# Optimization experiments

Hardware: AMD Instinct MI355X
Metric: run time of the kernel (lower is better)

Reference implementation:

```python
import jax, jax.numpy as jnp
import numpy as np

N_ROI, N_GRAPHS, HID, EDIM, EMB, NGRP = 116, 128, 64, 5, 16, 4
IN_CH, OUT_CH, N_LAYERS = 116, 2, 2


def _seg_softmax(scores, seg, num_segments):
    # numerically stable softmax over edges grouped by target node
    m = jax.ops.segment_max(scores, seg, num_segments=num_segments)
    ex = jnp.exp(scores - m[seg])
    s = jax.ops.segment_sum(ex, seg, num_segments=num_segments)
    return ex / (s[seg] + 1e-16)


def setup_inputs():
    key = jax.random.key(0)
    ks = jax.random.split(key, 16)
    N = N_ROI * N_GRAPHS
    idx = np.arange(N_ROI)
    s = np.repeat(idx, N_ROI)
    d = np.tile(idx, N_ROI)
    off = (np.arange(N_GRAPHS) * N_ROI)[:, None]
    src = (s[None, :] + off).reshape(-1)
    dst = (d[None, :] + off).reshape(-1)
    E = src.size

    def W(i, shp):
        fan = shp[-2] if len(shp) >= 2 else shp[-1]
        return jax.random.normal(ks[i], shp, jnp.float32) / np.sqrt(fan)

    def z(*shp):
        return jnp.zeros(shp, jnp.float32)

    return {
        "x": jax.random.normal(ks[0], (N, IN_CH), jnp.float32),
        "edge_attr": jax.random.normal(ks[1], (E, EDIM), jnp.float32),
        "emb": W(2, (NGRP, EMB)),
        "enc_W": W(3, (IN_CH + EMB, HID)), "enc_b": z(HID),
        "bn_g": jnp.ones((HID,), jnp.float32), "bn_b": z(HID),
        "gine_We": W(4, (EDIM, HID)), "gine_be": z(HID),
        "gine_W1": W(5, (HID, HID)), "gine_b1": z(HID),
        "gine_W2": W(6, (HID, HID)), "gine_b2": z(HID),
        "gat_Wl": W(7, (N_LAYERS, HID, HID)), "gat_bl": z(N_LAYERS, HID),
        "gat_Wr": W(8, (N_LAYERS, HID, HID)), "gat_br": z(N_LAYERS, HID),
        "gat_att": W(9, (N_LAYERS, HID)),
        "gat_We": W(10, (N_LAYERS, EDIM, HID)),
        "gat_bias": z(N_LAYERS, HID),
        "pool_W1": W(11, (HID, HID)), "pool_b1": z(HID), "pool_w2": W(12, (HID,)),
        "lin1_W": W(13, (HID, IN_CH)), "lin1_b": z(IN_CH),
        "lin2_W": W(14, (IN_CH, OUT_CH)), "lin2_b": z(OUT_CH),
        "edge_index": jnp.asarray(np.stack([src, dst]), jnp.int32),
        "batch": jnp.asarray(np.repeat(np.arange(N_GRAPHS), N_ROI), jnp.int32),
        "group_ids": jnp.asarray(np.tile(idx // 29, N_GRAPHS), jnp.int32),
        "num_graphs": N_GRAPHS,
    }


def reference(x, edge_attr, emb, enc_W, enc_b, bn_g, bn_b,
              gine_We, gine_be, gine_W1, gine_b1, gine_W2, gine_b2,
              gat_Wl, gat_bl, gat_Wr, gat_br, gat_att, gat_We, gat_bias,
              pool_W1, pool_b1, pool_w2, lin1_W, lin1_b, lin2_W, lin2_b,
              edge_index, batch, group_ids, num_graphs):
    src, dst = edge_index[0], edge_index[1]
    N = x.shape[0]
    # BrainEncodeEmbed: concat group embedding, linear, batchnorm (batch stats)
    h = jnp.concatenate([x, emb[group_ids]], axis=-1)          # [N, IN_CH+EMB]
    h = jax.nn.relu(h @ enc_W + enc_b)                          # [N, HID]
    mu = h.mean(0)
    var = h.var(0)
    h = (h - mu) * jax.lax.rsqrt(var + 1e-5) * bn_g + bn_b
    # GINEConv (eps=0): sum_j relu(x_j + lin_edge(e_ij)), then MLP
    e = edge_attr @ gine_We + gine_be                           # [E, HID]
    agg = jax.ops.segment_sum(jax.nn.relu(h[src] + e), dst, num_segments=N)
    h = h + agg
    h = jax.nn.relu(h @ gine_W1 + gine_b1) @ gine_W2 + gine_b2
    h = jax.nn.relu(h)
    # GATv2 layers (heads=1, concat=False)
    for l in range(N_LAYERS):
        xl = h @ gat_Wl[l] + gat_bl[l]                          # [N, HID]
        xr = h @ gat_Wr[l] + gat_br[l]
        zed = jax.nn.leaky_relu(xl[src] + xr[dst] + edge_attr @ gat_We[l], 0.2)
        alpha = _seg_softmax(zed @ gat_att[l], dst, N)          # [E]
        h = jax.nn.relu(
            jax.ops.segment_sum(xl[src] * alpha[:, None], dst, num_segments=N)
            + gat_bias[l])
    # AttentionPooling: global softmax over all nodes, scatter-add by graph
    w = jax.nn.softmax(jnp.tanh(h @ pool_W1 + pool_b1) @ pool_w2, axis=0)
    pooled = jax.ops.segment_sum(h * w[:, None], batch, num_segments=num_graphs)
    return jax.nn.relu(pooled @ lin1_W + lin1_b) @ lin2_W + lin2_b
```

## Files before the change

kernel.cpp:

```cpp
#include <hip/hip_runtime.h>
#include <math.h>

#define R    116
#define R2   (116*116)
#define G    128
#define NN   (R*G)
#define HID  64
#define EDIM 5
#define INCH 116
#define EMBD 16

__device__ __forceinline__ float waveReduceSum(float v) {
#pragma unroll
    for (int m = 32; m >= 1; m >>= 1) v += __shfl_xor(v, m, 64);
    return v;
}

__device__ __forceinline__ float rlane(float v, int i) {
    return __int_as_float(__builtin_amdgcn_readlane(__float_as_int(v), i));
}

__global__ __launch_bounds__(256) void k_etr(
    const float* __restrict__ ea, float* __restrict__ eat) {
    int b = blockIdx.x;
    int g = b >> 4;
    int t = b & 15;
    int i0 = (t >> 2) << 5, j0 = (t & 3) << 5;
    int ni = min(32, R - i0), nj = min(32, R - j0);
    __shared__ float tile[32][165];
    const float* src = ea + ((size_t)(g*R + i0)*R + j0)*EDIM;
    int tot = ni * nj * EDIM;
    for (int idx = threadIdx.x; idx < tot; idx += 256) {
        int ii = idx / (nj*EDIM);
        int rem = idx - ii*(nj*EDIM);
        tile[ii][rem] = src[(size_t)ii*R*EDIM + rem];
    }
    __syncthreads();
    float* dst = eat + ((size_t)(g*R + j0)*R + i0)*EDIM;
    int tot2 = nj * ni * EDIM;
    for (int idx = threadIdx.x; idx < tot2; idx += 256) {
        int jj = idx / (ni*EDIM);
        int rem = idx - jj*(ni*EDIM);
        int ii = rem / EDIM, e = rem - ii*EDIM;
        dst[(size_t)jj*R*EDIM + rem] = tile[ii][jj*EDIM + e];
    }
}

__global__ __launch_bounds__(64) void k_prep(
    const float* __restrict__ We, const float* __restrict__ att,
    float* __restrict__ wepack, float* __restrict__ was2) {
    int l = blockIdx.x, c = threadIdx.x;
    const float* Wl = We + l*EDIM*HID;
    const float* al = att + l*HID;
    float g0=Wl[c], g1=Wl[64+c], g2=Wl[128+c], g3=Wl[192+c], g4=Wl[256+c];
    float at = al[c];
    float* wp = wepack + l*HID*8 + c*8;
    wp[0]=g0; wp[1]=g1; wp[2]=g2; wp[3]=g3; wp[4]=g4; wp[5]=at;
    wp[6]=0.f; wp[7]=0.f;
    float p0 = waveReduceSum(g0*at);
    float p1 = waveReduceSum(g1*at);
    float p2 = waveReduceSum(g2*at);
    float p3 = waveReduceSum(g3*at);
    float p4 = waveReduceSum(g4*at);
    if (c == 0) {
        float* ws = was2 + l*8;
        ws[0]=p0; ws[1]=p1; ws[2]=p2; ws[3]=p3; ws[4]=p4;
    }
}

__global__ __launch_bounds__(256) void k_encode(
    const float* __restrict__ x, const float* __restrict__ emb,
    const int* __restrict__ group_ids,
    const float* __restrict__ W, const float* __restrict__ bvec,
    float* __restrict__ h) {
    int w = threadIdx.x >> 6, lane = threadIdx.x & 63;
    int n = blockIdx.x*4 + w;
    __shared__ float xin[4][136];
    for (int idx = lane; idx < INCH; idx += 64) xin[w][idx] = x[(size_t)n*INCH + idx];
    if (lane < EMBD) xin[w][INCH + lane] = emb[group_ids[n]*EMBD + lane];
    float acc = bvec[lane];
#pragma unroll
    for (int k = 0; k < INCH + EMBD; k += 4) {
        float4 q = *(const float4*)&xin[w][k];
        acc = fmaf(q.x, W[(k  )*HID + lane], acc);
        acc = fmaf(q.y, W[(k+1)*HID + lane], acc);
        acc = fmaf(q.z, W[(k+2)*HID + lane], acc);
        acc = fmaf(q.w, W[(k+3)*HID + lane], acc);
    }
    h[(size_t)n*HID + lane] = fmaxf(acc, 0.f);
}

__global__ __launch_bounds__(256) void k_stats_partial(
    const float* __restrict__ h, float* __restrict__ partials) {
    int b = blockIdx.x;
    int tid = threadIdx.x;
    int c = tid & 63, r0 = tid >> 6;
    float s = 0.f, s2 = 0.f;
    int row0 = b*64;
#pragma unroll
    for (int k = 0; k < 16; ++k) {
        float v = h[(size_t)(row0 + r0 + 4*k)*HID + c];
        s += v; s2 += v*v;
    }
    __shared__ float ls[256], l2[256];
    ls[tid] = s; l2[tid] = s2;
    __syncthreads();
    if (tid < 64) {
        s  = ls[tid] + ls[tid+64] + ls[tid+128] + ls[tid+192];
        s2 = l2[tid] + l2[tid+64] + l2[tid+128] + l2[tid+192];
        partials[b*128 + tid]      = s;
        partials[b*128 + 64 + tid] = s2;
    }
}

__global__ __launch_bounds__(64) void k_stats_final(
    const float* __restrict__ partials, const float* __restrict__ gam,
    const float* __restrict__ bet, float* __restrict__ stats) {
    int c = threadIdx.x;
    float s = 0.f, s2 = 0.f;
    for (int b = 0; b < NN/64; ++b) {
        s  += partials[b*128 + c];
        s2 += partials[b*128 + 64 + c];
    }
    float mu  = s / (float)NN;
    float var = s2 / (float)NN - mu*mu;
    float rs  = rsqrtf(var + 1e-5f);
    float sc  = rs * gam[c];
    stats[c]      = sc;
    stats[64 + c] = bet[c] - mu*sc;
}

__global__ __launch_bounds__(256) void k_gine(
    const float* __restrict__ h, const float* __restrict__ stats,
    const float* __restrict__ eat,
    const float* __restrict__ We, const float* __restrict__ be,
    const float* __restrict__ W1, const float* __restrict__ b1,
    const float* __restrict__ W2, const float* __restrict__ b2,
    float* __restrict__ hout) {
    int b = blockIdx.x;
    int g = b & (G-1), chunk = b >> 7;
    int tid = threadIdx.x, w = tid >> 6, lane = tid & 63;
    int j = chunk*4 + w;
    __shared__ float eac[4][R*8];
    __shared__ float t1s[4][68];
    size_t hbase = (size_t)g*R*HID;
    float scv = stats[lane], shv = stats[64 + lane];
    const float* col = eat + (size_t)(g*R + j)*R*EDIM;
    for (int idx = lane; idx < R*EDIM; idx += 64) {
        int i = idx / EDIM, e = idx - i*EDIM;
        eac[w][i*8 + e] = col[idx];
    }
    float w0=We[lane], w1v=We[64+lane], w2v=We[128+lane],
          w3v=We[192+lane], w4v=We[256+lane], bec=be[lane];
    const float* hg = h + hbase;
    float agg = 0.f;
#pragma unroll 4
    for (int i = 0; i < R; ++i) {
        float4 q = *(const float4*)&eac[w][i*8];
        float q4 = eac[w][i*8 + 4];
        float hv = fmaf(hg[(size_t)i*HID + lane], scv, shv);
        float ew = bec;
        ew = fmaf(q.x, w0,  ew); ew = fmaf(q.y, w1v, ew);
        ew = fmaf(q.z, w2v, ew); ew = fmaf(q.w, w3v, ew);
        ew = fmaf(q4,  w4v, ew);
        agg += fmaxf(hv + ew, 0.f);
    }
    float h1 = fmaf(hg[(size_t)j*HID + lane], scv, shv) + agg;
    t1s[w][lane] = h1;
    float a1 = b1[lane];
#pragma unroll
    for (int k = 0; k < HID; k += 4) {
        float4 tq = *(const float4*)&t1s[w][k];
        a1 = fmaf(tq.x, W1[(k  )*HID + lane], a1);
        a1 = fmaf(tq.y, W1[(k+1)*HID + lane], a1);
        a1 = fmaf(tq.z, W1[(k+2)*HID + lane], a1);
        a1 = fmaf(tq.w, W1[(k+3)*HID + lane], a1);
    }
    t1s[w][lane] = fmaxf(a1, 0.f);
    float a2 = b2[lane];
#pragma unroll
    for (int k = 0; k < HID; k += 4) {
        float4 tq = *(const float4*)&t1s[w][k];
        a2 = fmaf(tq.x, W2[(k  )*HID + lane], a2);
        a2 = fmaf(tq.y, W2[(k+1)*HID + lane], a2);
        a2 = fmaf(tq.z, W2[(k+2)*HID + lane], a2);
        a2 = fmaf(tq.w, W2[(k+3)*HID + lane], a2);
    }
    hout[hbase + (size_t)j*HID + lane] = fmaxf(a2, 0.f);
}

__global__ __launch_bounds__(256) void k_xlxr(
    const float* __restrict__ h,
    const float* __restrict__ Wl, const float* __restrict__ bl,
    const float* __restrict__ Wr, const float* __restrict__ br,
    const float* __restrict__ att,
    float* __restrict__ xl, float* __restrict__ xr,
    float* __restrict__ axl, float* __restrict__ axr) {
    int w = threadIdx.x >> 6, lane = threadIdx.x & 63;
    int n = blockIdx.x*4 + w;
    __shared__ float hr[4][68];
    hr[w][lane] = h[(size_t)n*HID + lane];
    float aL = bl[lane], aR = br[lane];
#pragma unroll
    for (int k = 0; k < HID; k += 4) {
        float4 q = *(const float4*)&hr[w][k];
        aL = fmaf(q.x, Wl[(k  )*HID + lane], aL);
        aR = fmaf(q.x, Wr[(k  )*HID + lane], aR);
        aL = fmaf(q.y, Wl[(k+1)*HID + lane], aL);
        aR = fmaf(q.y, Wr[(k+1)*HID + lane], aR);
        aL = fmaf(q.z, Wl[(k+2)*HID + lane], aL);
        aR = fmaf(q.z, Wr[(k+2)*HID + lane], aR);
        aL = fmaf(q.w, Wl[(k+3)*HID + lane], aL);
        aR = fmaf(q.w, Wr[(k+3)*HID + lane], aR);
    }
    xl[(size_t)n*HID + lane] = aL;
    xr[(size_t)n*HID + lane] = aR;
    float at = att[lane];
    float pL = waveReduceSum(aL * at);
    float pR = waveReduceSum(aR * at);
    if (lane == 0) { axl[n] = pL; axr[n] = pR; }
}

__global__ __launch_bounds__(256) void k_gat(
    const float* __restrict__ xl, const float* __restrict__ xr,
    const float* __restrict__ axlg, const float* __restrict__ axrg,
    const float* __restrict__ eat, const float* __restrict__ wepack,
    const float* __restrict__ wasg, const float* __restrict__ bias,
    float* __restrict__ hout) {
    int b = blockIdx.x;
    int g = b & (G-1), chunk = b >> 7;
    int j0c = chunk*15, jcnt = min(15, R - j0c);
    int tid = threadIdx.x, w = tid >> 6, lane = tid & 63;
    __shared__ float xls[R][66];
    size_t hbase = (size_t)g*R*HID;
    for (int idx = tid; idx < R*HID; idx += 256)
        xls[idx>>6][idx&63] = xl[hbase + idx];
    float biasv = bias[lane];
    float wasv0 = wasg[0], wasv1 = wasg[1], wasv2 = wasg[2],
          wasv3 = wasg[3], wasv4 = wasg[4];
    bool vB = lane < (R - 64);
    int rb = vB ? (64 + lane) : lane;
    float axA = axlg[g*R + lane];
    float axB = axlg[g*R + rb];
    __syncthreads();

    for (int p = 0; p < 2; ++p) {
        int jj0 = w + 8*p, jj1 = w + 4 + 8*p;
        bool act0 = jj0 < jcnt, act1 = jj1 < jcnt;
        int j0 = j0c + (act0 ? jj0 : 0);
        int j1 = j0c + (act1 ? jj1 : 0);
        const float* c0 = eat + (size_t)(g*R + j0)*R*EDIM;
        const float* c1 = eat + (size_t)(g*R + j1)*R*EDIM;
        float e0A[5], e0B[5], e1A[5], e1B[5];
#pragma unroll
        for (int e = 0; e < 5; ++e) {
            e0A[e] = c0[lane*EDIM + e];  e0B[e] = c0[rb*EDIM + e];
            e1A[e] = c1[lane*EDIM + e];  e1B[e] = c1[rb*EDIM + e];
        }
        int xo0 = __builtin_amdgcn_readfirstlane(j0*HID);
        int xo1 = __builtin_amdgcn_readfirstlane(j1*HID);
        const float* xr0 = xr + hbase + xo0;
        const float* xr1 = xr + hbase + xo1;
        float axr0 = axrg[g*R + j0];
        float axr1 = axrg[g*R + j1];
        float acc0A=0.f, acc0B=0.f, acc1A=0.f, acc1B=0.f;
#pragma unroll 4
        for (int c = 0; c < HID; c += 2) {
            float2 xA2 = *(const float2*)&xls[lane][c];
            float2 xB2 = *(const float2*)&xls[rb][c];
            const float* wpa = wepack + c*8;
            const float* wpb = wepack + (c+1)*8;
            float u0a = xr0[c], u0b = xr0[c+1];
            float u1a = xr1[c], u1b = xr1[c+1];
            {
                float zA = xA2.x + u0a;
                zA = fmaf(e0A[0],wpa[0],zA); zA = fmaf(e0A[1],wpa[1],zA);
                zA = fmaf(e0A[2],wpa[2],zA); zA = fmaf(e0A[3],wpa[3],zA);
                zA = fmaf(e0A[4],wpa[4],zA);
                acc0A = fmaf(__builtin_fabsf(zA), wpa[5], acc0A);
                float zB = xB2.x + u0a;
                zB = fmaf(e0B[0],wpa[0],zB); zB = fmaf(e0B[1],wpa[1],zB);
                zB = fmaf(e0B[2],wpa[2],zB); zB = fmaf(e0B[3],wpa[3],zB);
                zB = fmaf(e0B[4],wpa[4],zB);
                acc0B = fmaf(__builtin_fabsf(zB), wpa[5], acc0B);
                float yA = xA2.x + u1a;
                yA = fmaf(e1A[0],wpa[0],yA); yA = fmaf(e1A[1],wpa[1],yA);
                yA = fmaf(e1A[2],wpa[2],yA); yA = fmaf(e1A[3],wpa[3],yA);
                yA = fmaf(e1A[4],wpa[4],yA);
                acc1A = fmaf(__builtin_fabsf(yA), wpa[5], acc1A);
                float yB = xB2.x + u1a;
                yB = fmaf(e1B[0],wpa[0],yB); yB = fmaf(e1B[1],wpa[1],yB);
                yB = fmaf(e1B[2],wpa[2],yB); yB = fmaf(e1B[3],wpa[3],yB);
                yB = fmaf(e1B[4],wpa[4],yB);
                acc1B = fmaf(__builtin_fabsf(yB), wpa[5], acc1B);
            }
            {
                float zA = xA2.y + u0b;
                zA = fmaf(e0A[0],wpb[0],zA); zA = fmaf(e0A[1],wpb[1],zA);
                zA = fmaf(e0A[2],wpb[2],zA); zA = fmaf(e0A[3],wpb[3],zA);
                zA = fmaf(e0A[4],wpb[4],zA);
                acc0A = fmaf(__builtin_fabsf(zA), wpb[5], acc0A);
                float zB = xB2.y + u0b;
                zB = fmaf(e0B[0],wpb[0],zB); zB = fmaf(e0B[1],wpb[1],zB);
                zB = fmaf(e0B[2],wpb[2],zB); zB = fmaf(e0B[3],wpb[3],zB);
                zB = fmaf(e0B[4],wpb[4],zB);
                acc0B = fmaf(__builtin_fabsf(zB), wpb[5], acc0B);
                float yA = xA2.y + u1b;
                yA = fmaf(e1A[0],wpb[0],yA); yA = fmaf(e1A[1],wpb[1],yA);
                yA = fmaf(e1A[2],wpb[2],yA); yA = fmaf(e1A[3],wpb[3],yA);
                yA = fmaf(e1A[4],wpb[4],yA);
                acc1A = fmaf(__builtin_fabsf(yA), wpb[5], acc1A);
                float yB = xB2.y + u1b;
                yB = fmaf(e1B[0],wpb[0],yB); yB = fmaf(e1B[1],wpb[1],yB);
                yB = fmaf(e1B[2],wpb[2],yB); yB = fmaf(e1B[3],wpb[3],yB);
                yB = fmaf(e1B[4],wpb[4],yB);
                acc1B = fmaf(__builtin_fabsf(yB), wpb[5], acc1B);
            }
        }
        float L0A = axA + axr0, L0B = axB + axr0;
        L0A = fmaf(e0A[0],wasv0,L0A); L0A = fmaf(e0A[1],wasv1,L0A);
        L0A = fmaf(e0A[2],wasv2,L0A); L0A = fmaf(e0A[3],wasv3,L0A);
        L0A = fmaf(e0A[4],wasv4,L0A);
        L0B = fmaf(e0B[0],wasv0,L0B); L0B = fmaf(e0B[1],wasv1,L0B);
        L0B = fmaf(e0B[2],wasv2,L0B); L0B = fmaf(e0B[3],wasv3,L0B);
        L0B = fmaf(e0B[4],wasv4,L0B);
        float L1A = axA + axr1, L1B = axB + axr1;
        L1A = fmaf(e1A[0],wasv0,L1A); L1A = fmaf(e1A[1],wasv1,L1A);
        L1A = fmaf(e1A[2],wasv2,L1A); L1A = fmaf(e1A[3],wasv3,L1A);
        L1A = fmaf(e1A[4],wasv4,L1A);
        L1B = fmaf(e1B[0],wasv0,L1B); L1B = fmaf(e1B[1],wasv1,L1B);
        L1B = fmaf(e1B[2],wasv2,L1B); L1B = fmaf(e1B[3],wasv3,L1B);
        L1B = fmaf(e1B[4],wasv4,L1B);
        float s0A = fmaf(0.4f, acc0A, 0.6f*L0A);
        float s0B = vB ? fmaf(0.4f, acc0B, 0.6f*L0B) : -1e30f;
        float m0 = fmaxf(s0A, s0B);
#pragma unroll
        for (int k = 32; k >= 1; k >>= 1) m0 = fmaxf(m0, __shfl_xor(m0, k, 64));
        float x0A = __expf(s0A - m0);
        float x0B = vB ? __expf(s0B - m0) : 0.f;
        float sm0 = x0A + x0B;
#pragma unroll
        for (int k = 32; k >= 1; k >>= 1) sm0 += __shfl_xor(sm0, k, 64);
        float inv0 = 1.f / (sm0 + 1e-16f);
        float p0A = x0A * inv0, p0B = x0B * inv0;

        float s1A = fmaf(0.4f, acc1A, 0.6f*L1A);
        float s1B = vB ? fmaf(0.4f, acc1B, 0.6f*L1B) : -1e30f;
        float m1 = fmaxf(s1A, s1B);
#pragma unroll
        for (int k = 32; k >= 1; k >>= 1) m1 = fmaxf(m1, __shfl_xor(m1, k, 64));
        float x1A = __expf(s1A - m1);
        float x1B = vB ? __expf(s1B - m1) : 0.f;
        float sm1 = x1A + x1B;
#pragma unroll
        for (int k = 32; k >= 1; k >>= 1) sm1 += __shfl_xor(sm1, k, 64);
        float inv1 = 1.f / (sm1 + 1e-16f);
        float p1A = x1A * inv1, p1B = x1B * inv1;

        float o0 = 0.f, o1 = 0.f;
#pragma unroll 8
        for (int i = 0; i < 64; ++i) {
            float xv = xls[i][lane];
            o0 = fmaf(rlane(p0A, i), xv, o0);
            o1 = fmaf(rlane(p1A, i), xv, o1);
        }
#pragma unroll 4
        for (int i = 0; i < R-64; ++i) {
            float xv = xls[64+i][lane];
            o0 = fmaf(rlane(p0B, i), xv, o0);
            o1 = fmaf(rlane(p1B, i), xv, o1);
        }
        if (act0) hout[hbase + (size_t)j0*HID + lane] = fmaxf(o0 + biasv, 0.f);
        if (act1) hout[hbase + (size_t)j1*HID + lane] = fmaxf(o1 + biasv, 0.f);
    }
}

__global__ __launch_bounds__(256) void k_pool_score(
    const float* __restrict__ h, const float* __restrict__ W1,
    const float* __restrict__ b1, const float* __restrict__ w2,
    float* __restrict__ scores) {
    int w = threadIdx.x >> 6, lane = threadIdx.x & 63;
    int n = blockIdx.x*4 + w;
    __shared__ float hr[4][68];
    hr[w][lane] = h[(size_t)n*HID + lane];
    float acc = b1[lane];
#pragma unroll
    for (int k = 0; k < HID; k += 4) {
        float4 q = *(const float4*)&hr[w][k];
        acc = fmaf(q.x, W1[(k  )*HID + lane], acc);
        acc = fmaf(q.y, W1[(k+1)*HID + lane], acc);
        acc = fmaf(q.z, W1[(k+2)*HID + lane], acc);
        acc = fmaf(q.w, W1[(k+3)*HID + lane], acc);
    }
    float p = tanhf(acc) * w2[lane];
    p = waveReduceSum(p);
    if (lane == 0) scores[n] = p;
}

__global__ __launch_bounds__(1024) void k_pool_reduce(
    const float* __restrict__ scores, float* __restrict__ ms) {
    __shared__ float red[1024];
    int tid = threadIdx.x;
    float m = -1e30f;
    for (int i = tid; i < NN; i += 1024) m = fmaxf(m, scores[i]);
    red[tid] = m;
    __syncthreads();
    for (int s = 512; s > 0; s >>= 1) {
        if (tid < s) red[tid] = fmaxf(red[tid], red[tid+s]);
        __syncthreads();
    }
    float mx = red[0];
    __syncthreads();
    float sum = 0.f;
    for (int i = tid; i < NN; i += 1024) sum += __expf(scores[i] - mx);
    red[tid] = sum;
    __syncthreads();
    for (int s = 512; s > 0; s >>= 1) {
        if (tid < s) red[tid] += red[tid+s];
        __syncthreads();
    }
    if (tid == 0) { ms[0] = mx; ms[1] = red[0]; }
}

__global__ __launch_bounds__(64) void k_pool_final(
    const float* __restrict__ h, const float* __restrict__ scores,
    const float* __restrict__ ms,
    const float* __restrict__ lin1W, const float* __restrict__ lin1b,
    const float* __restrict__ lin2W, const float* __restrict__ lin2b,
    float* __restrict__ out) {
    int g = blockIdx.x, c = threadIdx.x;
    float mx = ms[0], inv = 1.f / ms[1];
    float pc = 0.f;
    int nb = g*R;
    for (int r = 0; r < R; ++r) {
        float wv = __expf(scores[nb + r] - mx) * inv;
        pc = fmaf(h[(size_t)(nb + r)*HID + c], wv, pc);
    }
    __shared__ float pl[HID];
    __shared__ float t[INCH];
    pl[c] = pc;
    __syncthreads();
    for (int k = c; k < INCH; k += 64) {
        float acc = lin1b[k];
#pragma unroll 8
        for (int q = 0; q < HID; ++q) acc = fmaf(pl[q], lin1W[q*INCH + k], acc);
        t[k] = fmaxf(acc, 0.f);
    }
    __syncthreads();
    if (c < 2) {
        float o = lin2b[c];
        for (int k = 0; k < INCH; ++k) o = fmaf(t[k], lin2W[k*2 + c], o);
        out[g*2 + c] = o;
    }
}

extern "C" void kernel_launch(void* const* d_in, const int* in_sizes, int n_in,
                              void* d_out, int out_size, void* d_ws, size_t ws_size,
                              hipStream_t stream) {
    (void)in_sizes; (void)n_in; (void)out_size; (void)ws_size;
    const float* x        = (const float*)d_in[0];
    const float* edge_attr= (const float*)d_in[1];
    const float* emb      = (const float*)d_in[2];
    const float* enc_W    = (const float*)d_in[3];
    const float* enc_b    = (const float*)d_in[4];
    const float* bn_g     = (const float*)d_in[5];
    const float* bn_b     = (const float*)d_in[6];
    const float* gine_We  = (const float*)d_in[7];
    const float* gine_be  = (const float*)d_in[8];
    const float* gine_W1  = (const float*)d_in[9];
    const float* gine_b1  = (const float*)d_in[10];
    const float* gine_W2  = (const float*)d_in[11];
    const float* gine_b2  = (const float*)d_in[12];
    const float* gat_Wl   = (const float*)d_in[13];
    const float* gat_bl   = (const float*)d_in[14];
    const float* gat_Wr   = (const float*)d_in[15];
    const float* gat_br   = (const float*)d_in[16];
    const float* gat_att  = (const float*)d_in[17];
    const float* gat_We   = (const float*)d_in[18];
    const float* gat_bias = (const float*)d_in[19];
    const float* pool_W1  = (const float*)d_in[20];
    const float* pool_b1  = (const float*)d_in[21];
    const float* pool_w2  = (const float*)d_in[22];
    const float* lin1_W   = (const float*)d_in[23];
    const float* lin1_b   = (const float*)d_in[24];
    const float* lin2_W   = (const float*)d_in[25];
    const float* lin2_b   = (const float*)d_in[26];
    const int*   group_ids= (const int*)d_in[29];
    float* out = (float*)d_out;

    float* w = (float*)d_ws;
    float* eat      = w;
    float* hA       = eat + (size_t)R2*G*EDIM;
    float* hB       = hA + (size_t)NN*HID;
    float* xlb      = hB + (size_t)NN*HID;
    float* xrb      = xlb + (size_t)NN*HID;
    float* axl      = xrb + (size_t)NN*HID;
    float* axr      = axl + NN;
    float* scores   = axr + NN;
    float* partials = scores + NN;
    float* stats    = partials + (NN/64)*128;
    float* pms      = stats + 128;
    float* wepack   = pms + 2;
    float* was2     = wepack + 2*HID*8;

    k_etr<<<G*16, 256, 0, stream>>>(edge_attr, eat);
    k_prep<<<2, 64, 0, stream>>>(gat_We, gat_att, wepack, was2);
    k_encode<<<NN/4, 256, 0, stream>>>(x, emb, group_ids, enc_W, enc_b, hA);
    k_stats_partial<<<NN/64, 256, 0, stream>>>(hA, partials);
    k_stats_final<<<1, 64, 0, stream>>>(partials, bn_g, bn_b, stats);
    k_gine<<<G*29, 256, 0, stream>>>(hA, stats, eat, gine_We, gine_be,
                                     gine_W1, gine_b1, gine_W2, gine_b2, hB);
    k_xlxr<<<NN/4, 256, 0, stream>>>(hB, gat_Wl, gat_bl, gat_Wr, gat_br,
                                     gat_att, xlb, xrb, axl, axr);
    k_gat<<<G*8, 256, 0, stream>>>(xlb, xrb, axl, axr, eat, wepack,
                                   was2, gat_bias, hA);
    k_xlxr<<<NN/4, 256, 0, stream>>>(hA, gat_Wl + HID*HID, gat_bl + HID,
                                     gat_Wr + HID*HID, gat_br + HID,
                                     gat_att + HID, xlb, xrb, axl, axr);
    k_gat<<<G*8, 256, 0, stream>>>(xlb, xrb, axl, axr, eat, wepack + HID*8,
                                   was2 + 8, gat_bias + HID, hB);
    k_pool_score<<<NN/4, 256, 0, stream>>>(hB, pool_W1, pool_b1, pool_w2, scores);
    k_pool_reduce<<<1, 1024, 0, stream>>>(scores, pms);
    k_pool_final<<<G, 64, 0, stream>>>(hB, scores, pms, lin1_W, lin1_b,
                                       lin2_W, lin2_b, out);
}
```

Before: 258.6 us.

## Fuse per-node projections into GINE and GAT epilogues, widen GAT blocks

Folds the GATv2 xl/xr projections and attention dot products into the epilogue of the GINE kernel and the first GAT kernel, and folds the pooling score computation into the second GAT kernel. This removes three standalone per-node kernels and their global read of h. GAT blocks move from 256 to 512 threads, with each wave handling two targets in one pass instead of looping. Double-buffered xl/xr arrays avoid read/write hazards between layers, at the cost of more workspace and register pressure in the fused kernels.

```diff
diff --git a/kernel.cpp b/kernel.cpp
--- a/kernel.cpp
+++ b/kernel.cpp
@@ -130,13 +130,18 @@
     stats[64 + c] = bet[c] - mu*sc;
 }
 
-__global__ __launch_bounds__(256) void k_gine(
+__global__ __launch_bounds__(256) void k_gine_x(
     const float* __restrict__ h, const float* __restrict__ stats,
     const float* __restrict__ eat,
     const float* __restrict__ We, const float* __restrict__ be,
     const float* __restrict__ W1, const float* __restrict__ b1,
     const float* __restrict__ W2, const float* __restrict__ b2,
-    float* __restrict__ hout) {
+    float* __restrict__ hout,
+    const float* __restrict__ Wl, const float* __restrict__ bl,
+    const float* __restrict__ Wr, const float* __restrict__ br,
+    const float* __restrict__ att,
+    float* __restrict__ oxl, float* __restrict__ oxr,
+    float* __restrict__ oaxl, float* __restrict__ oaxr) {
     int b = blockIdx.x;
     int g = b & (G-1), chunk = b >> 7;
     int tid = threadIdx.x, w = tid >> 6, lane = tid & 63;
@@ -186,24 +191,13 @@
         a2 = fmaf(tq.z, W2[(k+2)*HID + lane], a2);
         a2 = fmaf(tq.w, W2[(k+3)*HID + lane], a2);
     }
-    hout[hbase + (size_t)j*HID + lane] = fmaxf(a2, 0.f);
-}
-
-__global__ __launch_bounds__(256) void k_xlxr(
-    const float* __restrict__ h,
-    const float* __restrict__ Wl, const float* __restrict__ bl,
-    const float* __restrict__ Wr, const float* __restrict__ br,
-    const float* __restrict__ att,
-    float* __restrict__ xl, float* __restrict__ xr,
-    float* __restrict__ axl, float* __restrict__ axr) {
-    int w = threadIdx.x >> 6, lane = threadIdx.x & 63;
-    int n = blockIdx.x*4 + w;
-    __shared__ float hr[4][68];
-    hr[w][lane] = h[(size_t)n*HID + lane];
+    float hr = fmaxf(a2, 0.f);
+    hout[hbase + (size_t)j*HID + lane] = hr;
+    t1s[w][lane] = hr;
     float aL = bl[lane], aR = br[lane];
 #pragma unroll
     for (int k = 0; k < HID; k += 4) {
-        float4 q = *(const float4*)&hr[w][k];
+        float4 q = *(const float4*)&t1s[w][k];
         aL = fmaf(q.x, Wl[(k  )*HID + lane], aL);
         aR = fmaf(q.x, Wr[(k  )*HID + lane], aR);
         aL = fmaf(q.y, Wl[(k+1)*HID + lane], aL);
@@ -213,27 +207,35 @@
         aL = fmaf(q.w, Wl[(k+3)*HID + lane], aL);
         aR = fmaf(q.w, Wr[(k+3)*HID + lane], aR);
     }
-    xl[(size_t)n*HID + lane] = aL;
-    xr[(size_t)n*HID + lane] = aR;
+    oxl[hbase + (size_t)j*HID + lane] = aL;
+    oxr[hbase + (size_t)j*HID + lane] = aR;
     float at = att[lane];
     float pL = waveReduceSum(aL * at);
     float pR = waveReduceSum(aR * at);
-    if (lane == 0) { axl[n] = pL; axr[n] = pR; }
-}
-
-__global__ __launch_bounds__(256) void k_gat(
+    if (lane == 0) { oaxl[g*R + j] = pL; oaxr[g*R + j] = pR; }
+}
+
+template<int MODE>
+__global__ __launch_bounds__(512) void k_gat_x(
     const float* __restrict__ xl, const float* __restrict__ xr,
     const float* __restrict__ axlg, const float* __restrict__ axrg,
     const float* __restrict__ eat, const float* __restrict__ wepack,
     const float* __restrict__ wasg, const float* __restrict__ bias,
-    float* __restrict__ hout) {
+    float* __restrict__ hout,
+    const float* __restrict__ WA, const float* __restrict__ bA,
+    const float* __restrict__ WB, const float* __restrict__ bB,
+    const float* __restrict__ attv,
+    float* __restrict__ oxl, float* __restrict__ oxr,
+    float* __restrict__ oaxl, float* __restrict__ oaxr,
+    float* __restrict__ oscores) {
     int b = blockIdx.x;
     int g = b & (G-1), chunk = b >> 7;
     int j0c = chunk*15, jcnt = min(15, R - j0c);
     int tid = threadIdx.x, w = tid >> 6, lane = tid & 63;
     __shared__ float xls[R][66];
+    __shared__ float tt[8][68];
     size_t hbase = (size_t)g*R*HID;
-    for (int idx = tid; idx < R*HID; idx += 256)
+    for (int idx = tid; idx < R*HID; idx += 512)
         xls[idx>>6][idx&63] = xl[hbase + idx];
     float biasv = bias[lane];
     float wasv0 = wasg[0], wasv1 = wasg[1], wasv2 = wasg[2],
@@ -244,157 +246,177 @@
     float axB = axlg[g*R + rb];
     __syncthreads();
 
-    for (int p = 0; p < 2; ++p) {
-        int jj0 = w + 8*p, jj1 = w + 4 + 8*p;
-        bool act0 = jj0 < jcnt, act1 = jj1 < jcnt;
-        int j0 = j0c + (act0 ? jj0 : 0);
-        int j1 = j0c + (act1 ? jj1 : 0);
-        const float* c0 = eat + (size_t)(g*R + j0)*R*EDIM;
-        const float* c1 = eat + (size_t)(g*R + j1)*R*EDIM;
-        float e0A[5], e0B[5], e1A[5], e1B[5];
-#pragma unroll
-        for (int e = 0; e < 5; ++e) {
-            e0A[e] = c0[lane*EDIM + e];  e0B[e] = c0[rb*EDIM + e];
-            e1A[e] = c1[lane*EDIM + e];  e1B[e] = c1[rb*EDIM + e];
+    int jj0 = w, jj1 = w + 8;
+    bool act0 = jj0 < jcnt, act1 = jj1 < jcnt;
+    int j0 = j0c + (act0 ? jj0 : 0);
+    int j1 = j0c + (act1 ? jj1 : 0);
+    const float* c0 = eat + (size_t)(g*R + j0)*R*EDIM;
+    const float* c1 = eat + (size_t)(g*R + j1)*R*EDIM;
+    float e0A[5], e0B[5], e1A[5], e1B[5];
+#pragma unroll
+    for (int e = 0; e < 5; ++e) {
+        e0A[e] = c0[lane*EDIM + e];  e0B[e] = c0[rb*EDIM + e];
+        e1A[e] = c1[lane*EDIM + e];  e1B[e] = c1[rb*EDIM + e];
+    }
+    int xo0 = __builtin_amdgcn_readfirstlane(j0*HID);
+    int xo1 = __builtin_amdgcn_readfirstlane(j1*HID);
+    const float* xr0 = xr + hbase + xo0;
+    const float* xr1 = xr + hbase + xo1;
+    float axr0 = axrg[g*R + j0];
+    float axr1 = axrg[g*R + j1];
+    float acc0A=0.f, acc0B=0.f, acc1A=0.f, acc1B=0.f;
+#pragma unroll 4
+    for (int c = 0; c < HID; c += 2) {
+        float2 xA2 = *(const float2*)&xls[lane][c];
+        float2 xB2 = *(const float2*)&xls[rb][c];
+        const float* wpa = wepack + c*8;
+        const float* wpb = wepack + (c+1)*8;
+        float u0a = xr0[c], u0b = xr0[c+1];
+        float u1a = xr1[c], u1b = xr1[c+1];
+        {
+            float zA = xA2.x + u0a;
+            zA = fmaf(e0A[0],wpa[0],zA); zA = fmaf(e0A[1],wpa[1],zA);
+            zA = fmaf(e0A[2],wpa[2],zA); zA = fmaf(e0A[3],wpa[3],zA);
+            zA = fmaf(e0A[4],wpa[4],zA);
+            acc0A = fmaf(__builtin_fabsf(zA), wpa[5], acc0A);
+            float zB = xB2.x + u0a;
+            zB = fmaf(e0B[0],wpa[0],zB); zB = fmaf(e0B[1],wpa[1],zB);
+            zB = fmaf(e0B[2],wpa[2],zB); zB = fmaf(e0B[3],wpa[3],zB);
+            zB = fmaf(e0B[4],wpa[4],zB);
+            acc0B = fmaf(__builtin_fabsf(zB), wpa[5], acc0B);
+            float yA = xA2.x + u1a;
+            yA = fmaf(e1A[0],wpa[0],yA); yA = fmaf(e1A[1],wpa[1],yA);
+            yA = fmaf(e1A[2],wpa[2],yA); yA = fmaf(e1A[3],wpa[3],yA);
+            yA = fmaf(e1A[4],wpa[4],yA);
+            acc1A = fmaf(__builtin_fabsf(yA), wpa[5], acc1A);
+            float yB = xB2.x + u1a;
+            yB = fmaf(e1B[0],wpa[0],yB); yB = fmaf(e1B[1],wpa[1],yB);
+            yB = fmaf(e1B[2],wpa[2],yB); yB = fmaf(e1B[3],wpa[3],yB);
+            yB = fmaf(e1B[4],wpa[4],yB);
+            acc1B = fmaf(__builtin_fabsf(yB), wpa[5], acc1B);
         }
-        int xo0 = __builtin_amdgcn_readfirstlane(j0*HID);
-        int xo1 = __builtin_amdgcn_readfirstlane(j1*HID);
-        const float* xr0 = xr + hbase + xo0;
-        const float* xr1 = xr + hbase + xo1;
-        float axr0 = axrg[g*R + j0];
-        float axr1 = axrg[g*R + j1];
-        float acc0A=0.f, acc0B=0.f, acc1A=0.f, acc1B=0.f;
+        {
+            float zA = xA2.y + u0b;
+            zA = fmaf(e0A[0],wpb[0],zA); zA = fmaf(e0A[1],wpb[1],zA);
+            zA = fmaf(e0A[2],wpb[2],zA); zA = fmaf(e0A[3],wpb[3],zA);
+            zA = fmaf(e0A[4],wpb[4],zA);
+            acc0A = fmaf(__builtin_fabsf(zA), wpb[5], acc0A);
+            float zB = xB2.y + u0b;
+            zB = fmaf(e0B[0],wpb[0],zB); zB = fmaf(e0B[1],wpb[1],zB);
+            zB = fmaf(e0B[2],wpb[2],zB); zB = fmaf(e0B[3],wpb[3],zB);
+            zB = fmaf(e0B[4],wpb[4],zB);
+            acc0B = fmaf(__builtin_fabsf(zB), wpb[5], acc0B);
+            float yA = xA2.y + u1b;
+            yA = fmaf(e1A[0],wpb[0],yA); yA = fmaf(e1A[1],wpb[1],yA);
+            yA = fmaf(e1A[2],wpb[2],yA); yA = fmaf(e1A[3],wpb[3],yA);
+            yA = fmaf(e1A[4],wpb[4],yA);
+            acc1A = fmaf(__builtin_fabsf(yA), wpb[5], acc1A);
+            float yB = xB2.y + u1b;
+            yB = fmaf(e1B[0],wpb[0],yB); yB = fmaf(e1B[1],wpb[1],yB);
+            yB = fmaf(e1B[2],wpb[2],yB); yB = fmaf(e1B[3],wpb[3],yB);
+            yB = fmaf(e1B[4],wpb[4],yB);
+            acc1B = fmaf(__builtin_fabsf(yB), wpb[5], acc1B);
+        }
+    }
+    float L0A = axA + axr0, L0B = axB + axr0;
+    L0A = fmaf(e0A[0],wasv0,L0A); L0A = fmaf(e0A[1],wasv1,L0A);
+    L0A = fmaf(e0A[2],wasv2,L0A); L0A = fmaf(e0A[3],wasv3,L0A);
+    L0A = fmaf(e0A[4],wasv4,L0A);
+    L0B = fmaf(e0B[0],wasv0,L0B); L0B = fmaf(e0B[1],wasv1,L0B);
+    L0B = fmaf(e0B[2],wasv2,L0B); L0B = fmaf(e0B[3],wasv3,L0B);
+    L0B = fmaf(e0B[4],wasv4,L0B);
+    float L1A = axA + axr1, L1B = axB + axr1;
+    L1A = fmaf(e1A[0],wasv0,L1A); L1A = fmaf(e1A[1],wasv1,L1A);
+    L1A = fmaf(e1A[2],wasv2,L1A); L1A = fmaf(e1A[3],wasv3,L1A);
+    L1A = fmaf(e1A[4],wasv4,L1A);
+    L1B = fmaf(e1B[0],wasv0,L1B); L1B = fmaf(e1B[1],wasv1,L1B);
+    L1B = fmaf(e1B[2],wasv2,L1B); L1B = fmaf(e1B[3],wasv3,L1B);
+    L1B = fmaf(e1B[4],wasv4,L1B);
+    float s0A = fmaf(0.4f, acc0A, 0.6f*L0A);
+    float s0B = vB ? fmaf(0.4f, acc0B, 0.6f*L0B) : -1e30f;
+    float m0 = fmaxf(s0A, s0B);
+#pragma unroll
+    for (int k = 32; k >= 1; k >>= 1) m0 = fmaxf(m0, __shfl_xor(m0, k, 64));
+    float x0A = __expf(s0A - m0);
+    float x0B = vB ? __expf(s0B - m0) : 0.f;
+    float sm0 = x0A + x0B;
+#pragma unroll
+    for (int k = 32; k >= 1; k >>= 1) sm0 += __shfl_xor(sm0, k, 64);
+    float inv0 = 1.f / (sm0 + 1e-16f);
+    float p0A = x0A * inv0, p0B = x0B * inv0;
+
+    float s1A = fmaf(0.4f, acc1A, 0.6f*L1A);
+    float s1B = vB ? fmaf(0.4f, acc1B, 0.6f*L1B) : -1e30f;
+    float m1 = fmaxf(s1A, s1B);
+#pragma unroll
+    for (int k = 32; k >= 1; k >>= 1) m1 = fmaxf(m1, __shfl_xor(m1, k, 64));
+    float x1A = __expf(s1A - m1);
+    float x1B = vB ? __expf(s1B - m1) : 0.f;
+    float sm1 = x1A + x1B;
+#pragma unroll
+    for (int k = 32; k >= 1; k >>= 1) sm1 += __shfl_xor(sm1, k, 64);
+    float inv1 = 1.f / (sm1 + 1e-16f);
+    float p1A = x1A * inv1, p1B = x1B * inv1;
+
+    float o0 = 0.f, o1 = 0.f;
+#pragma unroll 8
+    for (int i = 0; i < 64; ++i) {
+        float xv = xls[i][lane];
+        o0 = fmaf(rlane(p0A, i), xv, o0);
+        o1 = fmaf(rlane(p1A, i), xv, o1);
+    }
 #pragma unroll 4
-        for (int c = 0; c < HID; c += 2) {
-            float2 xA2 = *(const float2*)&xls[lane][c];
-            float2 xB2 = *(const float2*)&xls[rb][c];
-            const float* wpa = wepack + c*8;
-            const float* wpb = wepack + (c+1)*8;
-            float u0a = xr0[c], u0b = xr0[c+1];
-            float u1a = xr1[c], u1b = xr1[c+1];
-            {
-                float zA = xA2.x + u0a;
-                zA = fmaf(e0A[0],wpa[0],zA); zA = fmaf(e0A[1],wpa[1],zA);
-                zA = fmaf(e0A[2],wpa[2],zA); zA = fmaf(e0A[3],wpa[3],zA);
-                zA = fmaf(e0A[4],wpa[4],zA);
-                acc0A = fmaf(__builtin_fabsf(zA), wpa[5], acc0A);
-                float zB = xB2.x + u0a;
-                zB = fmaf(e0B[0],wpa[0],zB); zB = fmaf(e0B[1],wpa[1],zB);
-                zB = fmaf(e0B[2],wpa[2],zB); zB = fmaf(e0B[3],wpa[3],zB);
-                zB = fmaf(e0B[4],wpa[4],zB);
-                acc0B = fmaf(__builtin_fabsf(zB), wpa[5], acc0B);
-                float yA = xA2.x + u1a;
-                yA = fmaf(e1A[0],wpa[0],yA); yA = fmaf(e1A[1],wpa[1],yA);
-                yA = fmaf(e1A[2],wpa[2],yA); yA = fmaf(e1A[3],wpa[3],yA);
-                yA = fmaf(e1A[4],wpa[4],yA);
-                acc1A = fmaf(__builtin_fabsf(yA), wpa[5], acc1A);
-                float yB = xB2.x + u1a;
-                yB = fmaf(e1B[0],wpa[0],yB); yB = fmaf(e1B[1],wpa[1],yB);
-                yB = fmaf(e1B[2],wpa[2],yB); yB = fmaf(e1B[3],wpa[3],yB);
-                yB = fmaf(e1B[4],wpa[4],yB);
-                acc1B = fmaf(__builtin_fabsf(yB), wpa[5], acc1B);
+    for (int i = 0; i < R-64; ++i) {
+        float xv = xls[64+i][lane];
+        o0 = fmaf(rlane(p0B, i), xv, o0);
+        o1 = fmaf(rlane(p1B, i), xv, o1);
+    }
+    float hr0 = fmaxf(o0 + biasv, 0.f);
+    float hr1 = fmaxf(o1 + biasv, 0.f);
+
+#pragma unroll
+    for (int t = 0; t < 2; ++t) {
+        bool act = t ? act1 : act0;
+        if (!act) continue;
+        int j = t ? j1 : j0;
+        float hr = t ? hr1 : hr0;
+        hout[hbase + (size_t)j*HID + lane] = hr;
+        tt[w][lane] = hr;
+        if (MODE == 0) {
+            float aL = bA[lane], aR = bB[lane];
+#pragma unroll
+            for (int k = 0; k < HID; k += 4) {
+                float4 q = *(const float4*)&tt[w][k];
+                aL = fmaf(q.x, WA[(k  )*HID + lane], aL);
+                aR = fmaf(q.x, WB[(k  )*HID + lane], aR);
+                aL = fmaf(q.y, WA[(k+1)*HID + lane], aL);
+                aR = fmaf(q.y, WB[(k+1)*HID + lane], aR);
+                aL = fmaf(q.z, WA[(k+2)*HID + lane], aL);
+                aR = fmaf(q.z, WB[(k+2)*HID + lane], aR);
+                aL = fmaf(q.w, WA[(k+3)*HID + lane], aL);
+                aR = fmaf(q.w, WB[(k+3)*HID + lane], aR);
             }
-            {
-                float zA = xA2.y + u0b;
-                zA = fmaf(e0A[0],wpb[0],zA); zA = fmaf(e0A[1],wpb[1],zA);
-                zA = fmaf(e0A[2],wpb[2],zA); zA = fmaf(e0A[3],wpb[3],zA);
-                zA = fmaf(e0A[4],wpb[4],zA);
-                acc0A = fmaf(__builtin_fabsf(zA), wpb[5], acc0A);
-                float zB = xB2.y + u0b;
-                zB = fmaf(e0B[0],wpb[0],zB); zB = fmaf(e0B[1],wpb[1],zB);
-                zB = fmaf(e0B[2],wpb[2],zB); zB = fmaf(e0B[3],wpb[3],zB);
-                zB = fmaf(e0B[4],wpb[4],zB);
-                acc0B = fmaf(__builtin_fabsf(zB), wpb[5], acc0B);
-                float yA = xA2.y + u1b;
-                yA = fmaf(e1A[0],wpb[0],yA); yA = fmaf(e1A[1],wpb[1],yA);
-                yA = fmaf(e1A[2],wpb[2],yA); yA = fmaf(e1A[3],wpb[3],yA);
-                yA = fmaf(e1A[4],wpb[4],yA);
-                acc1A = fmaf(__builtin_fabsf(yA), wpb[5], acc1A);
-                float yB = xB2.y + u1b;
-                yB = fmaf(e1B[0],wpb[0],yB); yB = fmaf(e1B[1],wpb[1],yB);
-                yB = fmaf(e1B[2],wpb[2],yB); yB = fmaf(e1B[3],wpb[3],yB);
-                yB = fmaf(e1B[4],wpb[4],yB);
-                acc1B = fmaf(__builtin_fabsf(yB), wpb[5], acc1B);
+            oxl[hbase + (size_t)j*HID + lane] = aL;
+            oxr[hbase + (size_t)j*HID + lane] = aR;
+            float at = attv[lane];
+            float pL = waveReduceSum(aL * at);
+            float pR = waveReduceSum(aR * at);
+            if (lane == 0) { oaxl[g*R + j] = pL; oaxr[g*R + j] = pR; }
+        } else {
+            float acc = bA[lane];
+#pragma unroll
+            for (int k = 0; k < HID; k += 4) {
+                float4 q = *(const float4*)&tt[w][k];
+                acc = fmaf(q.x, WA[(k  )*HID + lane], acc);
+                acc = fmaf(q.y, WA[(k+1)*HID + lane], acc);
+                acc = fmaf(q.z, WA[(k+2)*HID + lane], acc);
+                acc = fmaf(q.w, WA[(k+3)*HID + lane], acc);
             }
+            float p = tanhf(acc) * attv[lane];
+            p = waveReduceSum(p);
+            if (lane == 0) oscores[g*R + j] = p;
         }
-        float L0A = axA + axr0, L0B = axB + axr0;
-        L0A = fmaf(e0A[0],wasv0,L0A); L0A = fmaf(e0A[1],wasv1,L0A);
-        L0A = fmaf(e0A[2],wasv2,L0A); L0A = fmaf(e0A[3],wasv3,L0A);
-        L0A = fmaf(e0A[4],wasv4,L0A);
-        L0B = fmaf(e0B[0],wasv0,L0B); L0B = fmaf(e0B[1],wasv1,L0B);
-        L0B = fmaf(e0B[2],wasv2,L0B); L0B = fmaf(e0B[3],wasv3,L0B);
-        L0B = fmaf(e0B[4],wasv4,L0B);
-        float L1A = axA + axr1, L1B = axB + axr1;
-        L1A = fmaf(e1A[0],wasv0,L1A); L1A = fmaf(e1A[1],wasv1,L1A);
-        L1A = fmaf(e1A[2],wasv2,L1A); L1A = fmaf(e1A[3],wasv3,L1A);
-        L1A = fmaf(e1A[4],wasv4,L1A);
-        L1B = fmaf(e1B[0],wasv0,L1B); L1B = fmaf(e1B[1],wasv1,L1B);
-        L1B = fmaf(e1B[2],wasv2,L1B); L1B = fmaf(e1B[3],wasv3,L1B);
-        L1B = fmaf(e1B[4],wasv4,L1B);
-        float s0A = fmaf(0.4f, acc0A, 0.6f*L0A);
-        float s0B = vB ? fmaf(0.4f, acc0B, 0.6f*L0B) : -1e30f;
-        float m0 = fmaxf(s0A, s0B);
-#pragma unroll
-        for (int k = 32; k >= 1; k >>= 1) m0 = fmaxf(m0, __shfl_xor(m0, k, 64));
-        float x0A = __expf(s0A - m0);
-        float x0B = vB ? __expf(s0B - m0) : 0.f;
-        float sm0 = x0A + x0B;
-#pragma unroll
-        for (int k = 32; k >= 1; k >>= 1) sm0 += __shfl_xor(sm0, k, 64);
-        float inv0 = 1.f / (sm0 + 1e-16f);
-        float p0A = x0A * inv0, p0B = x0B * inv0;
-
-        float s1A = fmaf(0.4f, acc1A, 0.6f*L1A);
-        float s1B = vB ? fmaf(0.4f, acc1B, 0.6f*L1B) : -1e30f;
-        float m1 = fmaxf(s1A, s1B);
-#pragma unroll
-        for (int k = 32; k >= 1; k >>= 1) m1 = fmaxf(m1, __shfl_xor(m1, k, 64));
-        float x1A = __expf(s1A - m1);
-        float x1B = vB ? __expf(s1B - m1) : 0.f;
-        float sm1 = x1A + x1B;
-#pragma unroll
-        for (int k = 32; k >= 1; k >>= 1) sm1 += __shfl_xor(sm1, k, 64);
-        float inv1 = 1.f / (sm1 + 1e-16f);
-        float p1A = x1A * inv1, p1B = x1B * inv1;
-
-        float o0 = 0.f, o1 = 0.f;
-#pragma unroll 8
-        for (int i = 0; i < 64; ++i) {
-            float xv = xls[i][lane];
-            o0 = fmaf(rlane(p0A, i), xv, o0);
-            o1 = fmaf(rlane(p1A, i), xv, o1);
-        }
-#pragma unroll 4
-        for (int i = 0; i < R-64; ++i) {
-            float xv = xls[64+i][lane];
-            o0 = fmaf(rlane(p0B, i), xv, o0);
-            o1 = fmaf(rlane(p1B, i), xv, o1);
-        }
-        if (act0) hout[hbase + (size_t)j0*HID + lane] = fmaxf(o0 + biasv, 0.f);
-        if (act1) hout[hbase + (size_t)j1*HID + lane] = fmaxf(o1 + biasv, 0.f);
-    }
-}
-
-__global__ __launch_bounds__(256) void k_pool_score(
-    const float* __restrict__ h, const float* __restrict__ W1,
-    const float* __restrict__ b1, const float* __restrict__ w2,
-    float* __restrict__ scores) {
-    int w = threadIdx.x >> 6, lane = threadIdx.x & 63;
-    int n = blockIdx.x*4 + w;
-    __shared__ float hr[4][68];
-    hr[w][lane] = h[(size_t)n*HID + lane];
-    float acc = b1[lane];
-#pragma unroll
-    for (int k = 0; k < HID; k += 4) {
-        float4 q = *(const float4*)&hr[w][k];
-        acc = fmaf(q.x, W1[(k  )*HID + lane], acc);
-        acc = fmaf(q.y, W1[(k+1)*HID + lane], acc);
-        acc = fmaf(q.z, W1[(k+2)*HID + lane], acc);
-        acc = fmaf(q.w, W1[(k+3)*HID + lane], acc);
-    }
-    float p = tanhf(acc) * w2[lane];
-    p = waveReduceSum(p);
-    if (lane == 0) scores[n] = p;
+    }
 }
 
 __global__ __launch_bounds__(1024) void k_pool_reduce(
@@ -492,11 +514,15 @@
     float* eat      = w;
     float* hA       = eat + (size_t)R2*G*EDIM;
     float* hB       = hA + (size_t)NN*HID;
-    float* xlb      = hB + (size_t)NN*HID;
-    float* xrb      = xlb + (size_t)NN*HID;
-    float* axl      = xrb + (size_t)NN*HID;
-    float* axr      = axl + NN;
-    float* scores   = axr + NN;
+    float* xlA      = hB + (size_t)NN*HID;
+    float* xrA      = xlA + (size_t)NN*HID;
+    float* xlB      = xrA + (size_t)NN*HID;
+    float* xrB      = xlB + (size_t)NN*HID;
+    float* axlA     = xrB + (size_t)NN*HID;
+    float* axrA     = axlA + NN;
+    float* axlB     = axrA + NN;
+    float* axrB     = axlB + NN;
+    float* scores   = axrB + NN;
     float* partials = scores + NN;
     float* stats    = partials + (NN/64)*128;
     float* pms      = stats + 128;
@@ -508,18 +534,22 @@
     k_encode<<<NN/4, 256, 0, stream>>>(x, emb, group_ids, enc_W, enc_b, hA);
     k_stats_partial<<<NN/64, 256, 0, stream>>>(hA, partials);
     k_stats_final<<<1, 64, 0, stream>>>(partials, bn_g, bn_b, stats);
-    k_gine<<<G*29, 256, 0, stream>>>(hA, stats, eat, gine_We, gine_be,
-                                     gine_W1, gine_b1, gine_W2, gine_b2, hB);
-    k_xlxr<<<NN/4, 256, 0, stream>>>(hB, gat_Wl, gat_bl, gat_Wr, gat_br,
-                                     gat_att, xlb, xrb, axl, axr);
-    k_gat<<<G*8, 256, 0, stream>>>(xlb, xrb, axl, axr, eat, wepack,
-                                   was2, gat_bias, hA);
-    k_xlxr<<<NN/4, 256, 0, stream>>>(hA, gat_Wl + HID*HID, gat_bl + HID,
-                                     gat_Wr + HID*HID, gat_br + HID,
-                                     gat_att + HID, xlb, xrb, axl, axr);
-    k_gat<<<G*8, 256, 0, stream>>>(xlb, xrb, axl, axr, eat, wepack + HID*8,
-                                   was2 + 8, gat_bias + HID, hB);
-    k_pool_score<<<NN/4, 256, 0, stream>>>(hB, pool_W1, pool_b1, pool_w2, scores);
+    k_gine_x<<<G*29, 256, 0, stream>>>(hA, stats, eat, gine_We, gine_be,
+                                       gine_W1, gine_b1, gine_W2, gine_b2, hB,
+                                       gat_Wl, gat_bl, gat_Wr, gat_br, gat_att,
+                                       xlA, xrA, axlA, axrA);
+    k_gat_x<0><<<G*8, 512, 0, stream>>>(xlA, xrA, axlA, axrA, eat, wepack,
+                                        was2, gat_bias, hA,
+                                        gat_Wl + HID*HID, gat_bl + HID,
+                                        gat_Wr + HID*HID, gat_br + HID,
+                                        gat_att + HID,
+                                        xlB, xrB, axlB, axrB, scores);
+    k_gat_x<1><<<G*8, 512, 0, stream>>>(xlB, xrB, axlB, axrB, eat,
+                                        wepack + HID*8, was2 + 8,
+                                        gat_bias + HID, hB,
+                                        pool_W1, pool_b1, pool_W1, pool_b1,
+                                        pool_w2,
+                                        xlA, xrA, axlA, axrA, scores);
     k_pool_reduce<<<1, 1024, 0, stream>>>(scores, pms);
     k_pool_final<<<G, 64, 0, stream>>>(hB, scores, pms, lin1_W, lin1_b,
                                        lin2_W, lin2_b, out);
```

Result: faster. 242.5 us (-6.2%).
